# Kernel optimization log

Hardware: AMD Instinct MI355X
Metric: run time of the kernel (lower is better)

The kernel has to match this reference:

```python
import jax, jax.numpy as jnp
import numpy as np
from jax import lax

N, CI, CO, K, H, W_SP, M = 32, 256, 256, 3, 64, 64, 4
TAU = 1.0 / 30.0
PAD = 1  # spatial-preserving for k=3, stride=1, dilation=1


def setup_inputs() -> dict:
    key = jax.random.key(0)
    ks = jax.random.split(key, 6)
    # kaiming_normal fan_out for the kernel bank: fan_out = CO*K*K (per torch semantics on this 6D tensor layout)
    fan_out = CO * K * K
    std = np.sqrt(2.0 / fan_out)
    x = jax.random.normal(ks[0], (N, CI, H, W_SP), dtype=jnp.float32)
    Wbank = jax.random.normal(ks[1], (CO, M, CI, K, K), dtype=jnp.float32) * std
    Bbank = jnp.zeros((CO, M), dtype=jnp.float32)
    hid = CI // M  # att_fc hidden = in_channels // num_weights
    w1 = jax.random.normal(ks[2], (hid, CI), dtype=jnp.float32) * np.sqrt(1.0 / CI)
    b1 = jnp.zeros((hid,), dtype=jnp.float32)
    w2 = jax.random.normal(ks[3], (M, hid), dtype=jnp.float32) * np.sqrt(1.0 / hid)
    b2 = jnp.zeros((M,), dtype=jnp.float32)
    return {"x": x, "Wbank": Wbank, "Bbank": Bbank, "w1": w1, "b1": b1, "w2": w2, "b2": b2}


def reference(x, Wbank, Bbank, w1, b1, w2, b2):
    n, ci, h, w = x.shape
    co = Wbank.shape[0]
    # attention over kernels: global avg pool -> 1x1 conv MLP -> softmax(logits * tau)
    pooled = jnp.mean(x, axis=(2, 3))                      # N,Ci
    hmid = jax.nn.relu(pooled @ w1.T + b1)                 # N,hid
    logits = hmid @ w2.T + b2                              # N,M
    pi = jax.nn.softmax(logits * TAU, axis=1)              # N,M
    # per-sample aggregated kernels and biases
    wn = jnp.einsum("nm,omikl->noikl", pi, Wbank)          # N,Co,Ci,K,K
    bn = pi @ Bbank.T                                      # N,Co
    # batch-as-groups conv2d (spatial-preserving)
    xg = x.reshape(1, n * ci, h, w)
    wg = wn.reshape(n * co, ci, K, K)
    y = lax.conv_general_dilated(
        xg, wg,
        window_strides=(1, 1),
        padding=[(PAD, PAD), (PAD, PAD)],
        rhs_dilation=(1, 1),
        dimension_numbers=("NCHW", "OIHW", "NCHW"),
        feature_group_count=n,
    )
    y = y.reshape(n, co, h, w) + bn[:, :, None, None]
    return y
```

## Files before the change

kernel.cpp:

```cpp
#include <hip/hip_runtime.h>
#include <hip/hip_bf16.h>
#include <stdint.h>

typedef __bf16 bf16;
typedef __bf16 bf16x8 __attribute__((ext_vector_type(8)));
typedef float f32x4 __attribute__((ext_vector_type(4)));

#define TAU (1.0f/30.0f)

#define NB 32
#define CI 256
#define CO 256
#define HH 64
#define WW 64
#define HID 64

#define WN_ELEMS ((size_t)NB*8*9*16*512)
#define WN_BYTES (WN_ELEMS*2)
#define XB_ELEMS ((size_t)NB*32*64*64*8)
#define XB_BYTES (XB_ELEMS*2)

__device__ __forceinline__ void async16(void* lds_uniform_base, const void* g_perlane) {
  __builtin_amdgcn_global_load_lds(
      (const __attribute__((address_space(1))) uint32_t*)g_perlane,
      (__attribute__((address_space(3))) uint32_t*)lds_uniform_base, 16, 0, 0);
}

__global__ void cvt_pool_kernel(const float* __restrict__ x, bf16* __restrict__ xb,
                                float* __restrict__ pooled) {
  const int cg = blockIdx.x, n = blockIdx.y, tid = threadIdx.x;
  const float* base = x + ((size_t)n*CI + cg*8)*4096;
  bf16* ob = xb + ((size_t)n*32 + cg)*4096*8;
  float s[8];
#pragma unroll
  for (int j = 0; j < 8; ++j) s[j] = 0.f;
  for (int it = 0; it < 16; ++it) {
    int pos = it*256 + tid;
    bf16x8 o;
#pragma unroll
    for (int j = 0; j < 8; ++j) {
      float v = base[(size_t)j*4096 + pos];
      s[j] += v;
      o[j] = (bf16)v;
    }
    *(bf16x8*)(ob + (size_t)pos*8) = o;
  }
  __shared__ float red[4][8];
#pragma unroll
  for (int j = 0; j < 8; ++j)
#pragma unroll
    for (int off = 32; off; off >>= 1) s[j] += __shfl_xor(s[j], off);
  int wv = tid >> 6, lane = tid & 63;
  if (lane == 0)
#pragma unroll
    for (int j = 0; j < 8; ++j) red[wv][j] = s[j];
  __syncthreads();
  if (tid < 8) {
    float t = red[0][tid] + red[1][tid] + red[2][tid] + red[3][tid];
    pooled[n*CI + cg*8 + tid] = t * (1.0f/4096.0f);
  }
}

__global__ void attn_kernel(const float* __restrict__ pooled,
                            const float* __restrict__ w1, const float* __restrict__ b1,
                            const float* __restrict__ w2, const float* __restrict__ b2,
                            float* __restrict__ pi) {
  int n = blockIdx.x, h = threadIdx.x;
  __shared__ float hm[HID];
  __shared__ float lgs[4];
  const float* pr = pooled + n*CI;
  float s = b1[h];
  for (int c = 0; c < CI; ++c) s += pr[c] * w1[h*CI + c];
  hm[h] = s > 0.f ? s : 0.f;
  __syncthreads();
  if (h < 4) {
    float lg = b2[h];
    for (int k = 0; k < HID; ++k) lg += hm[k] * w2[h*HID + k];
    lgs[h] = lg * TAU;
  }
  __syncthreads();
  if (h == 0) {
    float mx = fmaxf(fmaxf(lgs[0], lgs[1]), fmaxf(lgs[2], lgs[3]));
    float e0 = expf(lgs[0]-mx), e1 = expf(lgs[1]-mx), e2 = expf(lgs[2]-mx), e3 = expf(lgs[3]-mx);
    float inv = 1.f / (e0+e1+e2+e3);
    pi[n*4+0] = e0*inv; pi[n*4+1] = e1*inv; pi[n*4+2] = e2*inv; pi[n*4+3] = e3*inv;
  }
}

__global__ void agg_kernel(const float* __restrict__ Wbank, const float* __restrict__ pi,
                           bf16* __restrict__ wn) {
  int wid = blockIdx.x * 4 + (threadIdx.x >> 6);
  int lane = threadIdx.x & 63;
  int c = wid / 144;
  int rem = wid - c*144;
  int kk = rem >> 4;
  int cbg = rem & 15;
  int co  = cbg*16 + (lane & 15);
  int ci0 = c*32 + (lane >> 4)*8;
  float w[4][8];
#pragma unroll
  for (int m = 0; m < 4; ++m)
#pragma unroll
    for (int j = 0; j < 8; ++j)
      w[m][j] = Wbank[(size_t)((co*4 + m)*256 + ci0 + j)*9 + kk];
  for (int n = 0; n < NB; ++n) {
    float p0 = pi[n*4+0], p1 = pi[n*4+1], p2 = pi[n*4+2], p3 = pi[n*4+3];
    bf16x8 o;
#pragma unroll
    for (int j = 0; j < 8; ++j)
      o[j] = (bf16)(p0*w[0][j] + p1*w[1][j] + p2*w[2][j] + p3*w[3][j]);
    *(bf16x8*)(wn + ((size_t)n*1152 + c*144 + kk*16 + cbg)*512 + lane*8) = o;
  }
}

#define XROWS 10
#define XW 66

__global__ __launch_bounds__(256, 2)
void conv_kernel(const bf16* __restrict__ xb, const bf16* __restrict__ wn,
                 const float* __restrict__ pi, const float* __restrict__ Bbank,
                 float* __restrict__ y) {
  __shared__ __align__(16) bf16 xs[4*XROWS*XW*8];
  __shared__ __align__(16) bf16 wa[9*4*512];
  __shared__ float bns[64];
  const int tid = threadIdx.x;
  const int wv = tid >> 6, lane = tid & 63;
  const int l = lane & 15, u = lane >> 4;
  const int hwb = blockIdx.x;
  const int cot = blockIdx.y;
  const int n   = blockIdx.z;
  const int h0 = hwb * 8;

  for (int i = tid; i < 4*XROWS*XW*8/8; i += 256) ((int4*)xs)[i] = int4{0,0,0,0};
  if (tid < 64) {
    int co = cot*64 + tid;
    bns[tid] = pi[n*4+0]*Bbank[co*4+0] + pi[n*4+1]*Bbank[co*4+1]
             + pi[n*4+2]*Bbank[co*4+2] + pi[n*4+3]*Bbank[co*4+3];
  }

  f32x4 acc[2][4][4];
#pragma unroll
  for (int o = 0; o < 2; ++o)
#pragma unroll
    for (int a = 0; a < 4; ++a)
#pragma unroll
      for (int b = 0; b < 4; ++b)
#pragma unroll
        for (int k = 0; k < 4; ++k) acc[o][a][b][k] = 0.f;

  const bf16* wnb = wn + (size_t)n * 1152 * 512;

  for (int c = 0; c < 8; ++c) {
    __syncthreads();
    {
      const bf16* seg = wnb + (size_t)c*144*512 + (size_t)(cot*4 + wv)*512 + lane*8;
#pragma unroll
      for (int kk = 0; kk < 9; ++kk)
        async16(&wa[kk*2048 + wv*512], seg + (size_t)kk*16*512);
    }
    {
      const bf16* xg = xb + ((size_t)(n*32 + c*4 + wv))*4096*8 + lane*8;
#pragma unroll
      for (int r = 0; r < XROWS; ++r) {
        int hp = h0 - 1 + r;
        if (hp >= 0 && hp < HH)
          async16(&xs[((wv*XROWS + r)*XW + 1)*8], xg + (size_t)hp*64*8);
      }
    }
    __syncthreads();
#pragma unroll
    for (int kx = 0; kx < 3; ++kx) {
      bf16x8 bfr[4][4];
#pragma unroll
      for (int rr = 0; rr < 4; ++rr)
#pragma unroll
        for (int f = 0; f < 4; ++f)
          bfr[rr][f] = *(const bf16x8*)(&xs[((u*XROWS + wv*2 + rr)*XW + f*16 + l + kx)*8]);
#pragma unroll
      for (int ky = 0; ky < 3; ++ky) {
        const int kk = ky*3 + kx;
#pragma unroll
        for (int cb = 0; cb < 4; ++cb) {
          bf16x8 afr = *(const bf16x8*)(&wa[kk*2048 + cb*512 + lane*8]);
#pragma unroll
          for (int o = 0; o < 2; ++o)
#pragma unroll
            for (int f = 0; f < 4; ++f)
              acc[o][cb][f] = __builtin_amdgcn_mfma_f32_16x16x32_bf16(afr, bfr[o+ky][f], acc[o][cb][f], 0, 0, 0);
        }
      }
    }
  }
#pragma unroll
  for (int o = 0; o < 2; ++o) {
    const int h = h0 + wv*2 + o;
#pragma unroll
    for (int cb = 0; cb < 4; ++cb) {
#pragma unroll
      for (int f = 0; f < 4; ++f) {
        const int wcol = f*16 + l;
#pragma unroll
        for (int r4 = 0; r4 < 4; ++r4) {
          const int col = cb*16 + u*4 + r4;
          y[(((size_t)n*CO + cot*64 + col)*HH + h)*WW + wcol] = acc[o][cb][f][r4] + bns[col];
        }
      }
    }
  }
}

extern "C" void kernel_launch(void* const* d_in, const int* in_sizes, int n_in,
                              void* d_out, int out_size, void* d_ws, size_t ws_size,
                              hipStream_t stream) {
  const float* x     = (const float*)d_in[0];
  const float* Wbank = (const float*)d_in[1];
  const float* Bbank = (const float*)d_in[2];
  const float* w1    = (const float*)d_in[3];
  const float* b1    = (const float*)d_in[4];
  const float* w2    = (const float*)d_in[5];
  const float* b2    = (const float*)d_in[6];
  float* y = (float*)d_out;

  bf16*  wn     = (bf16*)d_ws;
  bf16*  xb     = (bf16*)((char*)d_ws + WN_BYTES);
  float* pooled = (float*)((char*)d_ws + WN_BYTES + XB_BYTES);
  float* pi     = pooled + NB*CI;

  dim3 cg(32, NB);
  cvt_pool_kernel<<<cg, 256, 0, stream>>>(x, xb, pooled);
  attn_kernel<<<NB, HID, 0, stream>>>(pooled, w1, b1, w2, b2, pi);
  agg_kernel<<<288, 256, 0, stream>>>(Wbank, pi, wn);
  dim3 grid(8, 4, NB);
  conv_kernel<<<grid, 256, 0, stream>>>(xb, wn, pi, Bbank, y);
}
```

Measured before the change: 190.4 us.

## Double-buffer conv LDS tiles and swizzle block order across XCDs

The conv kernel now keeps two LDS buffers for the input tile and the weight tile. It issues the async global-to-LDS loads for the next channel chunk before computing the current one, so each iteration needs one barrier instead of two. The grid is flattened and remapped so that consecutive blocks on the same XCD work on the same sample, which should improve L2 reuse of its weights and inputs. The doubled LDS footprint forces launch bounds down to one block per CU, so the overlap that two resident blocks used to provide is lost.

```diff
diff --git a/kernel.cpp b/kernel.cpp
--- a/kernel.cpp
+++ b/kernel.cpp
@@ -115,23 +115,27 @@
 
 #define XROWS 10
 #define XW 66
-
-__global__ __launch_bounds__(256, 2)
+#define XS_E (4*XROWS*XW*8)
+#define WA_E (9*4*512)
+
+__global__ __launch_bounds__(256, 1)
 void conv_kernel(const bf16* __restrict__ xb, const bf16* __restrict__ wn,
                  const float* __restrict__ pi, const float* __restrict__ Bbank,
                  float* __restrict__ y) {
-  __shared__ __align__(16) bf16 xs[4*XROWS*XW*8];
-  __shared__ __align__(16) bf16 wa[9*4*512];
+  __shared__ __align__(16) bf16 xs[2][XS_E];
+  __shared__ __align__(16) bf16 wa[2][WA_E];
   __shared__ float bns[64];
   const int tid = threadIdx.x;
   const int wv = tid >> 6, lane = tid & 63;
   const int l = lane & 15, u = lane >> 4;
-  const int hwb = blockIdx.x;
-  const int cot = blockIdx.y;
-  const int n   = blockIdx.z;
+  const int flat = blockIdx.x;
+  const int wid = ((flat & 7) << 7) + (flat >> 3);
+  const int n   = wid >> 5;
+  const int hwb = (wid >> 2) & 7;
+  const int cot = wid & 3;
   const int h0 = hwb * 8;
 
-  for (int i = tid; i < 4*XROWS*XW*8/8; i += 256) ((int4*)xs)[i] = int4{0,0,0,0};
+  for (int i = tid; i < 2*XS_E/8; i += 256) ((int4*)xs)[i] = int4{0,0,0,0};
   if (tid < 64) {
     int co = cot*64 + tid;
     bns[tid] = pi[n*4+0]*Bbank[co*4+0] + pi[n*4+1]*Bbank[co*4+1]
@@ -149,25 +153,30 @@
         for (int k = 0; k < 4; ++k) acc[o][a][b][k] = 0.f;
 
   const bf16* wnb = wn + (size_t)n * 1152 * 512;
+  const bf16* xgb = xb + (size_t)n*32*4096*8 + lane*8;
+
+  auto STAGE = [&](int c, int b) {
+    const bf16* seg = wnb + (size_t)c*144*512 + (size_t)(cot*4 + wv)*512 + lane*8;
+#pragma unroll
+    for (int kk = 0; kk < 9; ++kk)
+      async16(&wa[b][kk*2048 + wv*512], seg + (size_t)kk*16*512);
+    const bf16* xg = xgb + (size_t)(c*4 + wv)*4096*8;
+#pragma unroll
+    for (int r = 0; r < XROWS; ++r) {
+      int hp = h0 - 1 + r;
+      if (hp >= 0 && hp < HH)
+        async16(&xs[b][((wv*XROWS + r)*XW + 1)*8], xg + (size_t)hp*64*8);
+    }
+  };
+
+  __syncthreads();
+  STAGE(0, 0);
 
   for (int c = 0; c < 8; ++c) {
     __syncthreads();
-    {
-      const bf16* seg = wnb + (size_t)c*144*512 + (size_t)(cot*4 + wv)*512 + lane*8;
-#pragma unroll
-      for (int kk = 0; kk < 9; ++kk)
-        async16(&wa[kk*2048 + wv*512], seg + (size_t)kk*16*512);
-    }
-    {
-      const bf16* xg = xb + ((size_t)(n*32 + c*4 + wv))*4096*8 + lane*8;
-#pragma unroll
-      for (int r = 0; r < XROWS; ++r) {
-        int hp = h0 - 1 + r;
-        if (hp >= 0 && hp < HH)
-          async16(&xs[((wv*XROWS + r)*XW + 1)*8], xg + (size_t)hp*64*8);
-      }
-    }
-    __syncthreads();
+    if (c < 7) STAGE(c + 1, (c + 1) & 1);
+    const bf16* xsb = xs[c & 1];
+    const bf16* wab = wa[c & 1];
 #pragma unroll
     for (int kx = 0; kx < 3; ++kx) {
       bf16x8 bfr[4][4];
@@ -175,13 +184,13 @@
       for (int rr = 0; rr < 4; ++rr)
 #pragma unroll
         for (int f = 0; f < 4; ++f)
-          bfr[rr][f] = *(const bf16x8*)(&xs[((u*XROWS + wv*2 + rr)*XW + f*16 + l + kx)*8]);
+          bfr[rr][f] = *(const bf16x8*)(&xsb[((u*XROWS + wv*2 + rr)*XW + f*16 + l + kx)*8]);
 #pragma unroll
       for (int ky = 0; ky < 3; ++ky) {
         const int kk = ky*3 + kx;
 #pragma unroll
         for (int cb = 0; cb < 4; ++cb) {
-          bf16x8 afr = *(const bf16x8*)(&wa[kk*2048 + cb*512 + lane*8]);
+          bf16x8 afr = *(const bf16x8*)(&wab[kk*2048 + cb*512 + lane*8]);
 #pragma unroll
           for (int o = 0; o < 2; ++o)
 #pragma unroll
@@ -230,6 +239,5 @@
   cvt_pool_kernel<<<cg, 256, 0, stream>>>(x, xb, pooled);
   attn_kernel<<<NB, HID, 0, stream>>>(pooled, w1, b1, w2, b2, pi);
   agg_kernel<<<288, 256, 0, stream>>>(Wbank, pi, wn);
-  dim3 grid(8, 4, NB);
-  conv_kernel<<<grid, 256, 0, stream>>>(xb, wn, pi, Bbank, y);
-}
+  conv_kernel<<<1024, 256, 0, stream>>>(xb, wn, pi, Bbank, y);
+}
```

After: 223.7 us. +17.5%, slower.
